# Optimization experiments

Measured on AMD Instinct MI355X. Metric: run time of the kernel, lower is better.

The kernel has to match this reference:

```python
import jax, jax.numpy as jnp
import numpy as np

DIM, M_DIM, FOURIER, KNN = 128, 16, 4, 32
EDGE_IN = 2 * FOURIER + 2 * DIM + 1  # 265


def silu(x):
    return x * jax.nn.sigmoid(x)


def setup_inputs() -> dict:
    key = jax.random.key(0)
    ks = jax.random.split(key, 12)
    b, n = 2, 4096

    def w(k, shape):
        return jax.random.normal(k, shape, dtype=jnp.float32) * 0.02

    return {
        "feats": jax.random.normal(ks[0], (b, n, DIM), dtype=jnp.float32),
        "coors": jax.random.normal(ks[1], (b, n, 3), dtype=jnp.float32) * 3.0,
        # edge_mlp: Linear(265, 530) -> SiLU -> Linear(530, 16) -> SiLU
        "We1": w(ks[2], (EDGE_IN, 2 * EDGE_IN)), "be1": jnp.zeros((2 * EDGE_IN,), jnp.float32),
        "We2": w(ks[3], (2 * EDGE_IN, M_DIM)), "be2": jnp.zeros((M_DIM,), jnp.float32),
        # coors_mlp: Linear(16, 64) -> SiLU -> Linear(64, 1)
        "Wc1": w(ks[4], (M_DIM, 4 * M_DIM)), "bc1": jnp.zeros((4 * M_DIM,), jnp.float32),
        "Wc2": w(ks[5], (4 * M_DIM, 1)), "bc2": jnp.zeros((1,), jnp.float32),
        # node_mlp: Linear(dim+16, 2*dim) -> SiLU -> Linear(2*dim, dim)
        "Wn1": w(ks[6], (DIM + M_DIM, 2 * DIM)), "bn1": jnp.zeros((2 * DIM,), jnp.float32),
        "Wn2": w(ks[7], (2 * DIM, DIM)), "bn2": jnp.zeros((DIM,), jnp.float32),
    }


def reference(feats, coors, We1, be1, We2, be2, Wc1, bc1, Wc2, bc2, Wn1, bn1, Wn2, bn2):
    b, n, d = feats.shape
    # pairwise relative coords and squared distance: (b, n, n, 3), (b, n, n)
    rel_coors = coors[:, :, None, :] - coors[:, None, :, :]
    rel_dist = jnp.sum(rel_coors ** 2, axis=-1)

    # k nearest neighbors (smallest distance)
    _, idx = jax.lax.top_k(-rel_dist, KNN)  # (b, n, K)
    rel_coors = jnp.take_along_axis(rel_coors, idx[..., None], axis=2)  # (b, n, K, 3)
    rel_dist = jnp.take_along_axis(rel_dist, idx, axis=2)[..., None]    # (b, n, K, 1)

    # fourier encode distance -> (b, n, K, 2*F + 1)
    scales = 2.0 ** jnp.arange(FOURIER, dtype=rel_dist.dtype)
    xs = rel_dist[..., None] / scales  # (b, n, K, 1, F)
    fe = jnp.concatenate([jnp.sin(xs), jnp.cos(xs), rel_dist[..., None]], axis=-1)
    rel_dist = fe.reshape(b, n, KNN, 2 * FOURIER + 1)

    bidx = jnp.arange(b)[:, None, None]
    feats_j = feats[bidx, idx]                                   # (b, n, K, d)
    feats_i = jnp.broadcast_to(feats[:, :, None, :], (b, n, KNN, d))

    edge_in = jnp.concatenate([feats_i, feats_j, rel_dist], axis=-1)  # (b, n, K, 265)
    m_ij = silu(silu(edge_in @ We1 + be1) @ We2 + be2)                # (b, n, K, m)

    coor_w = (silu(m_ij @ Wc1 + bc1) @ Wc2 + bc2)[..., 0]             # (b, n, K)
    coors_out = jnp.einsum('bij,bijc->bic', coor_w, rel_coors) + coors

    m_i = m_ij.sum(axis=2)                                            # (b, n, m)
    node_h = silu(jnp.concatenate([feats, m_i], axis=-1) @ Wn1 + bn1)
    node_out = node_h @ Wn2 + bn2 + feats
    return node_out, coors_out
```

## Files before the change

### kernel.cpp

```cpp
#include <hip/hip_runtime.h>
#include <hip/hip_bf16.h>
#include <stdint.h>

typedef __hip_bfloat16 bf16;

using sh8    = __attribute__((ext_vector_type(8)))  short;
using sh4    = __attribute__((ext_vector_type(4)))  short;
using us4    = __attribute__((ext_vector_type(4)))  unsigned short;
using f32x16 = __attribute__((ext_vector_type(16))) float;
using fx4    = __attribute__((ext_vector_type(4)))  float;
using i32x2  = __attribute__((ext_vector_type(2)))  int;

#define NN    4096
#define NODES 8192
#define DIM   128
#define MD    16
#define KNNK  32
#define H1N   530
#define CPAD  544
#define PROW  1088

#define OFF_W1AB 0
#define OFF_WE2A 8704
#define OFF_WC1A 17536
#define OFF_BE2  19584
#define OFF_BC1  19616
#define OFF_WC2  19744
#define OFF_BC2  19872
#define WIMG_SH  19880

__device__ __forceinline__ float b2f(bf16 x){ return __bfloat162float(x); }
__device__ __forceinline__ bf16  f2b(float x){ return __float2bfloat16(x); }
__device__ __forceinline__ float silu_f(float x){
    return x * __builtin_amdgcn_rcpf(1.f + __expf(-x));
}

__device__ __forceinline__ unsigned short f2us(float f){
    unsigned x = __float_as_uint(f);
    unsigned r = x + 0x7FFFu + ((x >> 16) & 1u);
    return (unsigned short)(r >> 16);
}
__device__ __forceinline__ float us2f(unsigned short u){
    return __uint_as_float(((unsigned)u) << 16);
}
__device__ __forceinline__ unsigned pkbf(float a, float b){
    __hip_bfloat162 v = __float22bfloat162_rn(make_float2(a, b));
    return *(unsigned*)&v;
}
__device__ __forceinline__ void plswap(unsigned &a, unsigned &b){
    i32x2 r = __builtin_amdgcn_permlane32_swap((int)a, (int)b, false, false);
    a = (unsigned)r[0]; b = (unsigned)r[1];
}
__device__ __forceinline__ sh8 mk8(unsigned a, unsigned b, unsigned c, unsigned d){
    union { unsigned u[4]; sh8 s; } x;
    x.u[0] = a; x.u[1] = b; x.u[2] = c; x.u[3] = d;
    return x.s;
}
__device__ __forceinline__ float ldconv(const void* p, int fl, size_t i){
    return fl ? ((const float*)p)[i] : b2f(((const bf16*)p)[i]);
}

struct Ptrs { const void* p[14]; int n[14]; };

__global__ __launch_bounds__(256) void detect_kernel(Ptrs ps, int* flags){
    int tn = blockIdx.x;
    const bf16* s = (const bf16*)ps.p[tn];
    int n = ps.n[tn]; if (n > 8192) n = 8192;
    int bad = 0;
    for (int i = threadIdx.x; i < n; i += 256){
        float v = b2f(s[i]);
        if (!(fabsf(v) <= 64.f)) bad = 1;
    }
    __shared__ int sbad;
    if (threadIdx.x == 0) sbad = 0;
    __syncthreads();
    if (bad) atomicOr(&sbad, 1);
    __syncthreads();
    if (threadIdx.x == 0) flags[tn] = sbad;
}

#define PREP_TOTAL 1340352
__global__ __launch_bounds__(256) void prep_all(Ptrs ps, const int* __restrict__ flags,
        unsigned short* __restrict__ gwimg, unsigned short* __restrict__ We1T,
        unsigned short* __restrict__ fBF,   float* __restrict__ coorsF,
        float* __restrict__ be1F,  float* __restrict__ Wn1F,
        float* __restrict__ bn1F,  float* __restrict__ Wn2F,
        float* __restrict__ bn2F,  float* __restrict__ coorsS){
    int gid = blockIdx.x * 256 + threadIdx.x;
    if (gid < 4352){
        int c = gid >> 3, f = gid & 7;
        gwimg[OFF_W1AB + gid] =
            (c < H1N) ? f2us(ldconv(ps.p[2], flags[2], (size_t)(256 + f) * H1N + c)) : 0;
    } else if (gid < 8704){
        int e = gid - 4352; int c = e >> 3, jj = e & 7;
        gwimg[OFF_W1AB + 4352 + e] =
            (jj == 0 && c < H1N) ? f2us(ldconv(ps.p[2], flags[2], (size_t)264 * H1N + c)) : 0;
    } else if (gid < 17536){
        int e = gid - 8704; int o = e / 552, c = e - o * 552;
        gwimg[OFF_WE2A + e] =
            (c < H1N) ? f2us(ldconv(ps.p[4], flags[4], (size_t)c * 16 + o)) : 0;
    } else if (gid < 19584){
        int e = gid - 17536; int u = e >> 5, k = e & 31;
        gwimg[OFF_WC1A + e] =
            (k < 16) ? f2us(ldconv(ps.p[6], flags[6], (size_t)k * 64 + u)) : 0;
    } else if (gid < 19600){
        ((float*)(gwimg + OFF_BE2))[gid - 19584] = ldconv(ps.p[5], flags[5], gid - 19584);
    } else if (gid < 19664){
        ((float*)(gwimg + OFF_BC1))[gid - 19600] = ldconv(ps.p[7], flags[7], gid - 19600);
    } else if (gid < 19728){
        ((float*)(gwimg + OFF_WC2))[gid - 19664] = ldconv(ps.p[8], flags[8], gid - 19664);
    } else if (gid < 19732){
        int z = gid - 19728;
        ((float*)(gwimg + OFF_BC2))[z] = (z == 0) ? ldconv(ps.p[9], flags[9], 0) : 0.f;
    } else if (gid >= 32768 && gid < 172032){
        int e = gid - 32768; int n = e >> 7, k = e & 127;
        float v;
        if (n < CPAD) v = (n < H1N) ? ldconv(ps.p[2], flags[2], (size_t)k * H1N + n) : 0.f;
        else { int n2 = n - CPAD;
               v = (n2 < H1N) ? ldconv(ps.p[2], flags[2], (size_t)(128 + k) * H1N + n2) : 0.f; }
        We1T[e] = f2us(v);
    } else if (gid >= 172032 && gid < 1220608){
        int e = gid - 172032;
        fBF[e] = f2us(ldconv(ps.p[0], flags[0], e));
    } else if (gid >= 1220608 && gid < 1245184){
        int e = gid - 1220608;
        coorsF[e] = ldconv(ps.p[1], flags[1], e);
    } else if (gid >= 1245184 && gid < 1245714){
        int e = gid - 1245184;
        be1F[e] = ldconv(ps.p[3], flags[3], e);
    } else if (gid >= 1245760 && gid < 1282624){
        int e = gid - 1245760;
        Wn1F[e] = ldconv(ps.p[10], flags[10], e);
    } else if (gid >= 1282624 && gid < 1282880){
        int e = gid - 1282624;
        bn1F[e] = ldconv(ps.p[11], flags[11], e);
    } else if (gid >= 1282880 && gid < 1315648){
        int e = gid - 1282880;
        Wn2F[e] = ldconv(ps.p[12], flags[12], e);
    } else if (gid >= 1315648 && gid < 1315776){
        int e = gid - 1315648;
        bn2F[e] = ldconv(ps.p[13], flags[13], e);
    } else if (gid >= 1315776 && gid < 1340352){
        int e = gid - 1315776;
        int n = e / 3, c = e - n * 3;
        coorsS[(size_t)c * NODES + n] = ldconv(ps.p[1], flags[1], e);
    }
}

__global__ __launch_bounds__(512, 6) void knn_kernel(const float* __restrict__ coorsS,
                                                     int* __restrict__ idx_out){
    __shared__ unsigned hist[8][1024];
    __shared__ unsigned long long blist[8][64];
    __shared__ int cntO[8], cntB[8];

    int t = threadIdx.x, lane = t & 63, wid = t >> 6;
    int node = (blockIdx.x << 3) + wid;
    int b = node >> 12, i = node & (NN - 1);
    const float* cx = coorsS + (size_t)b * NN;
    const float* cy = coorsS + NODES + (size_t)b * NN;
    const float* cz = coorsS + 2 * NODES + (size_t)b * NN;

    float qx = cx[i], qy = cy[i], qz = cz[i];

    unsigned* h = &hist[wid][0];
    {
        uint4* hz = (uint4*)h;
        uint4 z = make_uint4(0,0,0,0);
        #pragma unroll
        for (int zl = 0; zl < 4; ++zl) hz[zl * 64 + lane] = z;
    }
    if (lane == 0){ cntO[wid] = 0; cntB[wid] = 0; }
    asm volatile("" ::: "memory");

    for (int s = 0; s < 16; ++s){
        int j0 = (s << 8) + (lane << 2);
        fx4 X = *(const fx4*)(cx + j0);
        fx4 Y = *(const fx4*)(cy + j0);
        fx4 Z = *(const fx4*)(cz + j0);
        #pragma unroll
        for (int k = 0; k < 4; ++k){
            float dx = qx - X[k], dy = qy - Y[k], dz = qz - Z[k];
            float d  = dx*dx + dy*dy + dz*dz;
            float d2 = d * d;
            atomicAdd(&h[__float_as_uint(d2 * d2) >> 22], 1u);
        }
    }
    asm volatile("s_waitcnt lgkmcnt(0)" ::: "memory");

    unsigned S = 0;
    {
        uint4* hz = (uint4*)h;
        #pragma unroll
        for (int g = 0; g < 4; ++g){
            uint4 v = hz[lane * 4 + g];
            S += v.x + v.y + v.z + v.w;
        }
    }
    unsigned scan = S;
    #pragma unroll
    for (int off = 1; off < 64; off <<= 1){
        unsigned nv = __shfl_up(scan, off);
        if (lane >= off) scan += nv;
    }
    unsigned excl = scan - S;
    unsigned long long own = __ballot(excl < KNNK && excl + S >= KNNK);
    int src = __ffsll((unsigned long long)own) - 1;
    unsigned run = excl, Bloc = 0, below_l = 0;
    #pragma unroll
    for (int r = 0; r < 16; ++r){
        unsigned c = h[lane * 16 + r];
        if (run < KNNK && run + c >= KNNK){ Bloc = lane * 16 + r; below_l = run; }
        run += c;
    }
    unsigned B    = __shfl(Bloc, src);
    unsigned below= __shfl(below_l, src);
    unsigned need = KNNK - below;

    int* co = &cntO[wid];
    int* cbn = &cntB[wid];
    unsigned long long* bl = &blist[wid][0];
    for (int s = 0; s < 16; ++s){
        int j0 = (s << 8) + (lane << 2);
        fx4 X = *(const fx4*)(cx + j0);
        fx4 Y = *(const fx4*)(cy + j0);
        fx4 Z = *(const fx4*)(cz + j0);
        #pragma unroll
        for (int k = 0; k < 4; ++k){
            float dx = qx - X[k], dy = qy - Y[k], dz = qz - Z[k];
            float d  = dx*dx + dy*dy + dz*dz;
            float d2 = d * d;
            unsigned bk = __float_as_uint(d2 * d2) >> 22;
            int j = j0 + k;
            if (bk < B){
                int pos = atomicAdd(co, 1);
                idx_out[(size_t)node * KNNK + pos] = j;
            } else if (bk == B){
                unsigned long long mk = ((unsigned long long)__float_as_uint(d) << 32)
                                        | (unsigned)j;
                int p = atomicAdd(cbn, 1);
                if (p < 64) bl[p] = mk;
            }
        }
    }
    asm volatile("s_waitcnt lgkmcnt(0) vmcnt(0)" ::: "memory");
    int nb = *cbn;

    if (nb <= 64){
        unsigned long long e = (lane < nb) ? bl[lane] : ~0ull;
        for (unsigned r = 0; r < need; ++r){
            unsigned long long m = e;
            #pragma unroll
            for (int off = 32; off > 0; off >>= 1){
                unsigned long long o = __shfl_xor(m, off);
                if (o < m) m = o;
            }
            if (lane == 0)
                idx_out[(size_t)node * KNNK + below + r] = (int)(unsigned)(m & 0xffffffffull);
            if (e == m) e = ~0ull;
        }
    } else {
        unsigned long long lastk = 0;
        for (unsigned r = 0; r < need; ++r){
            unsigned long long lmin = ~0ull;
            for (int s = 0; s < 64; ++s){
                int j = (s << 6) + lane;
                float dx = qx - cx[j];
                float dy = qy - cy[j];
                float dz = qz - cz[j];
                float d  = dx*dx + dy*dy + dz*dz;
                float d2 = d * d;
                if ((__float_as_uint(d2 * d2) >> 22) == B){
                    unsigned long long mk = (((unsigned long long)__float_as_uint(d) << 32)
                                             | (unsigned)j) + 1ull;
                    if (mk > lastk && mk < lmin) lmin = mk;
                }
            }
            #pragma unroll
            for (int off = 32; off > 0; off >>= 1){
                unsigned long long o = __shfl_xor(lmin, off);
                if (o < lmin) lmin = o;
            }
            if (lane == 0)
                idx_out[(size_t)node * KNNK + below + r] =
                    (int)(unsigned)((lmin - 1ull) & 0xffffffffull);
            lastk = lmin;
        }
    }
}

__global__ __launch_bounds__(256) void p_gemm(const unsigned short* __restrict__ fBF,
                                              const unsigned short* __restrict__ We1T,
                                              const float* __restrict__ be1,
                                              unsigned short* __restrict__ P){
    int t = threadIdx.x, lane = t & 63, wid = t >> 6;
    int e31 = lane & 31, hi = lane >> 5;
    int mW = (blockIdx.x << 7) + (wid << 5);
    int n0 = blockIdx.y << 5;

    const unsigned short* Arow = fBF  + (size_t)(mW + e31) * DIM + hi * 8;
    const unsigned short* Brow = We1T + (size_t)(n0 + e31) * DIM + hi * 8;

    f32x16 acc = {0.f,0.f,0.f,0.f,0.f,0.f,0.f,0.f,0.f,0.f,0.f,0.f,0.f,0.f,0.f,0.f};
    #pragma unroll
    for (int kc = 0; kc < 8; ++kc){
        sh8 a  = *(const sh8*)(Arow + kc * 16);
        sh8 bv = *(const sh8*)(Brow + kc * 16);
        acc = __builtin_amdgcn_mfma_f32_32x32x16_bf16(a, bv, acc, 0, 0, 0);
    }
    int n = n0 + e31;
    float beadd = 0.f;
    if (n < CPAD) beadd = (n < H1N) ? be1[n] : 0.f;
    #pragma unroll
    for (int g = 0; g < 4; ++g)
        #pragma unroll
        for (int r = 0; r < 4; ++r){
            int m = mW + 8*g + 4*hi + r;
            P[(size_t)m * PROW + n] = f2us(acc[4*g + r] + beadd);
        }
}

__global__ __launch_bounds__(512, 6) void edge_kernel(
        const float* __restrict__ coors, const int* __restrict__ idx,
        const unsigned short* __restrict__ gw,
        const unsigned short* __restrict__ P,
        float* __restrict__ mi_out, void* __restrict__ dout,
        const int* __restrict__ flagp){
    __shared__ __align__(16) unsigned short sWe2[16 * 552];
    __shared__ __align__(16) unsigned short trans[8][1280];

    int t = threadIdx.x, lane = t & 63, wid = t >> 6;
    int gnode = (blockIdx.x << 3) + wid;
    int b = gnode >> 12;

    {
        const float4* s1 = (const float4*)(gw + OFF_WE2A);
        float4* d1 = (float4*)sWe2;
        for (int e = t; e < 1104; e += 512) d1[e] = s1[e];
    }

    const float* cb = coors + (size_t)b * NN * 3;
    int i = gnode & (NN - 1);
    float qx = cb[i*3+0], qy = cb[i*3+1], qz = cb[i*3+2];

    int e31 = lane & 31, hi = lane >> 5;
    int e15 = lane & 15, q  = lane >> 4;

    int jme = idx[(size_t)gnode * KNNK + e31];
    float rx = qx - cb[jme*3+0];
    float ry = qy - cb[jme*3+1];
    float rz = qz - cb[jme*3+2];
    float d = rx*rx + ry*ry + rz*rz;

    float s8v, c8v;
    __sincosf(d * 0.125f, &s8v, &c8v);
    float s4  = 2.f*s8v*c8v, c4  = 1.f - 2.f*s8v*s8v;
    float s2a = 2.f*s4*c4,   c2a = 1.f - 2.f*s4*s4;
    float s1a = 2.f*s2a*c2a, c1a = 1.f - 2.f*s2a*s2a;

    unsigned frb[9];
    frb[0] = f2us(s1a); frb[1] = f2us(s2a); frb[2] = f2us(s4); frb[3] = f2us(s8v);
    frb[4] = f2us(c1a); frb[5] = f2us(c2a); frb[6] = f2us(c4); frb[7] = f2us(c8v);
    frb[8] = f2us(d);

    sh8 bfragC;
    #pragma unroll
    for (int j = 0; j < 8; ++j)
        bfragC[j] = (hi == 0) ? (short)frb[j]
                  : (short)((j == 0) ? frb[8] : (j == 1) ? 0x3F80u : 0u);

    int nbase = gnode & ~(NN - 1);
    int j0 = __shfl(jme, lane >> 2);
    int j1 = __shfl(jme, 16 + (lane >> 2));
    const unsigned short* Pst0 = P + (size_t)(nbase + j0) * PROW + CPAD + (lane & 3) * 8;
    const unsigned short* Pst1 = P + (size_t)(nbase + j1) * PROW + CPAD + (lane & 3) * 8;
    const unsigned short* Pirow = P + (size_t)gnode * PROW;

    unsigned short* stg = &trans[wid][0];
    unsigned short* sw0 = stg + (lane >> 2) * 40 + (lane & 3) * 8;
    unsigned short* sw1 = stg + (16 + (lane >> 2)) * 40 + (lane & 3) * 8;

    const float* g_be2 = (const float*)(gw + OFF_BE2);
    const float* g_bc1 = (const float*)(gw + OFF_BC1);
    const float* g_wc2 = (const float*)(gw + OFF_WC2);
    const float* g_bc2 = (const float*)(gw + OFF_BC2);

    f32x16 accD = {0.f,0.f,0.f,0.f,0.f,0.f,0.f,0.f,
                   0.f,0.f,0.f,0.f,0.f,0.f,0.f,0.f};

    sh8 g0v = *(const sh8*)(Pst0);
    sh8 g1v = *(const sh8*)(Pst1);

    __syncthreads();

    #pragma unroll 1
    for (int ch = 0; ch < 17; ++ch){
        int c0 = ch * 32;
        *(sh8*)sw0 = g0v;
        *(sh8*)sw1 = g1v;
        if (ch < 16){
            g0v = *(const sh8*)(Pst0 + c0 + 32);
            g1v = *(const sh8*)(Pst1 + c0 + 32);
        }

        unsigned short piS = Pirow[c0 + e31];
        sh8 afrag = *(const sh8*)(gw + OFF_W1AB + (size_t)(hi * 544 + c0 + e31) * 8);
        afrag[1] = hi ? (short)piS : afrag[1];

        f32x16 cc;
        #pragma unroll
        for (int g = 0; g < 4; ++g){
            us4 pj = *(const us4*)(stg + e31 * 40 + 8*g + 4*hi);
            cc[4*g+0] = us2f(pj.x);
            cc[4*g+1] = us2f(pj.y);
            cc[4*g+2] = us2f(pj.z);
            cc[4*g+3] = us2f(pj.w);
        }
        f32x16 h = __builtin_amdgcn_mfma_f32_32x32x16_bf16(afrag, bfragC, cc, 0, 0, 0);

        unsigned u0 = pkbf(silu_f(h[0]),  silu_f(h[1]));
        unsigned u1 = pkbf(silu_f(h[2]),  silu_f(h[3]));
        unsigned u2 = pkbf(silu_f(h[4]),  silu_f(h[5]));
        unsigned u3 = pkbf(silu_f(h[6]),  silu_f(h[7]));
        unsigned u4 = pkbf(silu_f(h[8]),  silu_f(h[9]));
        unsigned u5 = pkbf(silu_f(h[10]), silu_f(h[11]));
        unsigned u6 = pkbf(silu_f(h[12]), silu_f(h[13]));
        unsigned u7 = pkbf(silu_f(h[14]), silu_f(h[15]));
        plswap(u0, u2); plswap(u1, u3);
        plswap(u4, u6); plswap(u5, u7);
        sh8 A1 = mk8(u0, u1, u2, u3);
        sh8 A2 = mk8(u4, u5, u6, u7);

        const unsigned short* wrow = &sWe2[(size_t)(e31 & 15) * 552 + c0 + (hi << 3)];
        sh8 B1 = *(const sh8*)(wrow);
        sh8 B2 = *(const sh8*)(wrow + 16);
        accD = __builtin_amdgcn_mfma_f32_32x32x16_bf16(A1, B1, accD, 0, 0, 0);
        accD = __builtin_amdgcn_mfma_f32_32x32x16_bf16(A2, B2, accD, 0, 0, 0);
    }

    float be2v = g_be2[e31 & 15];
    float mval[16];
    float msum = 0.f;
    #pragma unroll
    for (int r = 0; r < 16; ++r){
        mval[r] = silu_f(accD[r] + be2v);
        msum += mval[r];
    }
    msum += __shfl_xor(msum, 32);

    if (e31 < 16){
        #pragma unroll
        for (int r = 0; r < 16; ++r){
            int edge = (r & 3) + 8 * (r >> 2) + 4 * hi;
            stg[edge * 16 + e31] = f2us(mval[r]);
        }
        if (hi == 0)
            mi_out[(size_t)gnode * MD + e31] = msum;
    }

    float tsum0 = 0.f, tsum1 = 0.f;
    #pragma unroll
    for (int ut = 0; ut < 4; ++ut){
        sh8 wa3 = *(const sh8*)(gw + OFF_WC1A + (size_t)(ut * 16 + e15) * 32 + q * 8);
        sh8 b0  = (q < 2) ? *(const sh8*)&stg[e15 * 16 + q * 8]        : (sh8)0;
        sh8 b1  = (q < 2) ? *(const sh8*)&stg[(16 + e15) * 16 + q * 8] : (sh8)0;
        fx4 a0 = {0.f,0.f,0.f,0.f};
        fx4 a1 = {0.f,0.f,0.f,0.f};
        a0 = __builtin_amdgcn_mfma_f32_16x16x32_bf16(wa3, b0, a0, 0, 0, 0);
        a1 = __builtin_amdgcn_mfma_f32_16x16x32_bf16(wa3, b1, a1, 0, 0, 0);
        fx4 bc1q = *(const fx4*)&g_bc1[ut * 16 + q * 4];
        fx4 wcq  = *(const fx4*)&g_wc2[ut * 16 + q * 4];
        #pragma unroll
        for (int r = 0; r < 4; ++r){
            tsum0 += silu_f(a0[r] + bc1q[r]) * wcq[r];
            tsum1 += silu_f(a1[r] + bc1q[r]) * wcq[r];
        }
    }
    tsum0 += __shfl_xor(tsum0, 16); tsum0 += __shfl_xor(tsum0, 32);
    tsum1 += __shfl_xor(tsum1, 16); tsum1 += __shfl_xor(tsum1, 32);
    float cw = ((lane < 16) ? tsum0 : tsum1) + g_bc2[0];

    float en = (lane < 32) ? 1.f : 0.f;
    float cx = en * cw * rx, cy = en * cw * ry, cz = en * cw * rz;
    #pragma unroll
    for (int off = 1; off <= 32; off <<= 1){
        cx += __shfl_xor(cx, off);
        cy += __shfl_xor(cy, off);
        cz += __shfl_xor(cz, off);
    }
    if (lane == 0){
        size_t base = (size_t)NODES * DIM + (size_t)gnode * 3;
        if (*flagp){
            float* o = (float*)dout;
            o[base+0] = cx + qx; o[base+1] = cy + qy; o[base+2] = cz + qz;
        } else {
            bf16* o = (bf16*)dout;
            o[base+0] = f2b(cx + qx); o[base+1] = f2b(cy + qy); o[base+2] = f2b(cz + qz);
        }
    }
}

__global__ __launch_bounds__(256) void node_kernel(
        const void* __restrict__ featsRaw, const float* __restrict__ m_i,
        const float* __restrict__ Wn1,   const float* __restrict__ bn1,
        const float* __restrict__ Wn2,   const float* __restrict__ bn2,
        void* __restrict__ dout,         const int* __restrict__ flagp){
    __shared__ __align__(16) float X[8][144];
    __shared__ __align__(16) float Hs[8][256];
    int t = threadIdx.x;
    int g0 = blockIdx.x << 3;
    int fl = flagp[0];

    for (int e = t; e < 8 * DIM; e += 256){
        int nd = e >> 7, c = e & 127;
        size_t off = (size_t)(g0 + nd) * DIM + c;
        X[nd][c] = fl ? ((const float*)featsRaw)[off]
                      : b2f(((const bf16*)featsRaw)[off]);
    }
    if (t < 128){
        int nd = t >> 4, c = t & 15;
        X[nd][DIM + c] = m_i[(size_t)(g0 + nd) * MD + c];
    }
    __syncthreads();

    float acc[8] = {};
    for (int r4 = 0; r4 < 144; r4 += 4){
        float w0 = Wn1[(size_t)(r4+0) * 256 + t];
        float w1 = Wn1[(size_t)(r4+1) * 256 + t];
        float w2 = Wn1[(size_t)(r4+2) * 256 + t];
        float w3 = Wn1[(size_t)(r4+3) * 256 + t];
        #pragma unroll
        for (int nd = 0; nd < 8; ++nd){
            fx4 x4 = *(const fx4*)&X[nd][r4];
            acc[nd] += x4[0]*w0 + x4[1]*w1 + x4[2]*w2 + x4[3]*w3;
        }
    }
    float bb = bn1[t];
    #pragma unroll
    for (int nd = 0; nd < 8; ++nd) Hs[nd][t] = silu_f(acc[nd] + bb);
    __syncthreads();

    int c = t & 127, g = t >> 7;
    float a2[4] = {};
    for (int r4 = 0; r4 < 256; r4 += 4){
        float w0 = Wn2[(size_t)(r4+0) * DIM + c];
        float w1 = Wn2[(size_t)(r4+1) * DIM + c];
        float w2 = Wn2[(size_t)(r4+2) * DIM + c];
        float w3 = Wn2[(size_t)(r4+3) * DIM + c];
        #pragma unroll
        for (int u = 0; u < 4; ++u){
            fx4 h4 = *(const fx4*)&Hs[g*4 + u][r4];
            a2[u] += h4[0]*w0 + h4[1]*w1 + h4[2]*w2 + h4[3]*w3;
        }
    }
    float b2v = bn2[c];
    #pragma unroll
    for (int u = 0; u < 4; ++u){
        int nd = g*4 + u;
        float v = a2[u] + b2v + X[nd][c];
        size_t off2 = (size_t)(g0 + nd) * DIM + c;
        if (fl) ((float*)dout)[off2] = v;
        else    ((bf16*)dout)[off2]  = f2b(v);
    }
}

extern "C" void kernel_launch(void* const* d_in, const int* in_sizes, int n_in,
                              void* d_out, int out_size, void* d_ws, size_t ws_size,
                              hipStream_t stream){
    char* ws = (char*)d_ws;
    size_t off = 0;
    auto alloc = [&](size_t bytes) -> char* {
        off = (off + 511) & ~(size_t)511;
        char* p = ws + off;
        off += bytes;
        return p;
    };

    int* flags = (int*)alloc(14 * 4);
    unsigned short* gwimg = (unsigned short*)alloc((size_t)WIMG_SH * 2);
    unsigned short* We1T  = (unsigned short*)alloc((size_t)1088 * 128 * 2);
    unsigned short* fBF   = (unsigned short*)alloc((size_t)NODES * DIM * 2);
    float* coorsF = (float*)alloc((size_t)2 * NN * 3 * 4);
    float* be1F   = (float*)alloc((size_t)544 * 4);
    float* Wn1F   = (float*)alloc((size_t)144 * 256 * 4);
    float* bn1F   = (float*)alloc((size_t)256 * 4);
    float* Wn2F   = (float*)alloc((size_t)256 * 128 * 4);
    float* bn2F   = (float*)alloc((size_t)128 * 4);
    float* coorsS = (float*)alloc((size_t)3 * NODES * 4);
    int*   idx    = (int*)  alloc((size_t)NODES * KNNK * 4);
    unsigned short* P = (unsigned short*) alloc((size_t)NODES * PROW * 2);
    float* mi     = (float*)alloc((size_t)NODES * MD * 4);

    Ptrs ps;
    for (int i = 0; i < 14; ++i){ ps.p[i] = d_in[i]; ps.n[i] = in_sizes[i]; }

    detect_kernel<<<14, 256, 0, stream>>>(ps, flags);
    prep_all<<<(PREP_TOTAL + 255) / 256, 256, 0, stream>>>(
        ps, flags, gwimg, We1T, fBF, coorsF, be1F, Wn1F, bn1F, Wn2F, bn2F, coorsS);
    knn_kernel<<<NODES/8, 512, 0, stream>>>(coorsS, idx);
    p_gemm<<<dim3(64, 34), 256, 0, stream>>>(fBF, We1T, be1F, P);
    edge_kernel<<<NODES/8, 512, 0, stream>>>(coorsF, idx, gwimg, P, mi,
                                             d_out, flags + 0);
    node_kernel<<<1024, 256, 0, stream>>>(d_in[0], mi, Wn1F, bn1F, Wn2F, bn2F,
                                          d_out, flags + 0);
}
```

Measured before the change: 252.0 us.

## Merge knn with P-gemm and fuse node MLP into edge kernel

Folds the independent P-projection GEMM into the knn launch as extra blocks, so both run concurrently in one grid. It also fuses the node MLP into the edge kernel epilogue, keeping per-node message sums in shared memory instead of a global m_i buffer. Together these remove two launches and a global round trip. The cost is more shared memory and extra work per edge block, which may lower occupancy. The GEMM blocks also inherit the knn kernel's 512-thread launch bounds and shared-memory allocation.

```diff
diff --git a/kernel.cpp b/kernel.cpp
--- a/kernel.cpp
+++ b/kernel.cpp
@@ -147,14 +147,49 @@
     }
 }
 
-__global__ __launch_bounds__(512, 6) void knn_kernel(const float* __restrict__ coorsS,
-                                                     int* __restrict__ idx_out){
+__global__ __launch_bounds__(512, 6) void knn_pgemm(
+        const float* __restrict__ coorsS, int* __restrict__ idx_out,
+        const unsigned short* __restrict__ fBF,
+        const unsigned short* __restrict__ We1T,
+        const float* __restrict__ be1, unsigned short* __restrict__ P){
     __shared__ unsigned hist[8][1024];
     __shared__ unsigned long long blist[8][64];
     __shared__ int cntO[8], cntB[8];
 
+    int bid = blockIdx.x;
     int t = threadIdx.x, lane = t & 63, wid = t >> 6;
-    int node = (blockIdx.x << 3) + wid;
+    int e31 = lane & 31, hi = lane >> 5;
+
+    if (bid >= 1024){
+        int sub = bid - 1024;
+        int bx = sub & 63, by = sub >> 6;
+        int mW = (bx << 7) + ((wid & 3) << 5);
+        int n0 = (by << 6) + ((wid >> 2) << 5);
+
+        const unsigned short* Arow = fBF  + (size_t)(mW + e31) * DIM + hi * 8;
+        const unsigned short* Brow = We1T + (size_t)(n0 + e31) * DIM + hi * 8;
+
+        f32x16 acc = {0.f,0.f,0.f,0.f,0.f,0.f,0.f,0.f,0.f,0.f,0.f,0.f,0.f,0.f,0.f,0.f};
+        #pragma unroll
+        for (int kc = 0; kc < 8; ++kc){
+            sh8 a  = *(const sh8*)(Arow + kc * 16);
+            sh8 bv = *(const sh8*)(Brow + kc * 16);
+            acc = __builtin_amdgcn_mfma_f32_32x32x16_bf16(a, bv, acc, 0, 0, 0);
+        }
+        int n = n0 + e31;
+        float beadd = 0.f;
+        if (n < CPAD) beadd = (n < H1N) ? be1[n] : 0.f;
+        #pragma unroll
+        for (int g = 0; g < 4; ++g)
+            #pragma unroll
+            for (int r = 0; r < 4; ++r){
+                int m = mW + 8*g + 4*hi + r;
+                P[(size_t)m * PROW + n] = f2us(acc[4*g + r] + beadd);
+            }
+        return;
+    }
+
+    int node = (bid << 3) + wid;
     int b = node >> 12, i = node & (NN - 1);
     const float* cx = coorsS + (size_t)b * NN;
     const float* cy = coorsS + NODES + (size_t)b * NN;
@@ -288,54 +323,37 @@
     }
 }
 
-__global__ __launch_bounds__(256) void p_gemm(const unsigned short* __restrict__ fBF,
-                                              const unsigned short* __restrict__ We1T,
-                                              const float* __restrict__ be1,
-                                              unsigned short* __restrict__ P){
-    int t = threadIdx.x, lane = t & 63, wid = t >> 6;
-    int e31 = lane & 31, hi = lane >> 5;
-    int mW = (blockIdx.x << 7) + (wid << 5);
-    int n0 = blockIdx.y << 5;
-
-    const unsigned short* Arow = fBF  + (size_t)(mW + e31) * DIM + hi * 8;
-    const unsigned short* Brow = We1T + (size_t)(n0 + e31) * DIM + hi * 8;
-
-    f32x16 acc = {0.f,0.f,0.f,0.f,0.f,0.f,0.f,0.f,0.f,0.f,0.f,0.f,0.f,0.f,0.f,0.f};
-    #pragma unroll
-    for (int kc = 0; kc < 8; ++kc){
-        sh8 a  = *(const sh8*)(Arow + kc * 16);
-        sh8 bv = *(const sh8*)(Brow + kc * 16);
-        acc = __builtin_amdgcn_mfma_f32_32x32x16_bf16(a, bv, acc, 0, 0, 0);
-    }
-    int n = n0 + e31;
-    float beadd = 0.f;
-    if (n < CPAD) beadd = (n < H1N) ? be1[n] : 0.f;
-    #pragma unroll
-    for (int g = 0; g < 4; ++g)
-        #pragma unroll
-        for (int r = 0; r < 4; ++r){
-            int m = mW + 8*g + 4*hi + r;
-            P[(size_t)m * PROW + n] = f2us(acc[4*g + r] + beadd);
-        }
-}
-
-__global__ __launch_bounds__(512, 6) void edge_kernel(
+__global__ __launch_bounds__(512, 6) void edge_node(
         const float* __restrict__ coors, const int* __restrict__ idx,
         const unsigned short* __restrict__ gw,
         const unsigned short* __restrict__ P,
-        float* __restrict__ mi_out, void* __restrict__ dout,
-        const int* __restrict__ flagp){
+        const void* __restrict__ featsRaw,
+        const float* __restrict__ Wn1,  const float* __restrict__ bn1,
+        const float* __restrict__ Wn2,  const float* __restrict__ bn2,
+        void* __restrict__ dout,        const int* __restrict__ flagp){
     __shared__ __align__(16) unsigned short sWe2[16 * 552];
     __shared__ __align__(16) unsigned short trans[8][1280];
+    __shared__ __align__(16) float Xn[8][144];
+    __shared__ __align__(16) float Hsn[8][256];
 
     int t = threadIdx.x, lane = t & 63, wid = t >> 6;
     int gnode = (blockIdx.x << 3) + wid;
+    int gblk  = blockIdx.x << 3;
     int b = gnode >> 12;
+    int fl = flagp[0];
 
     {
         const float4* s1 = (const float4*)(gw + OFF_WE2A);
         float4* d1 = (float4*)sWe2;
         for (int e = t; e < 1104; e += 512) d1[e] = s1[e];
+    }
+    {
+        for (int e = t; e < 8 * DIM; e += 512){
+            int nd = e >> 7, c = e & 127;
+            size_t off = (size_t)(gblk + nd) * DIM + c;
+            Xn[nd][c] = fl ? ((const float*)featsRaw)[off]
+                           : b2f(((const bf16*)featsRaw)[off]);
+        }
     }
 
     const float* cb = coors + (size_t)b * NN * 3;
@@ -454,7 +472,7 @@
             stg[edge * 16 + e31] = f2us(mval[r]);
         }
         if (hi == 0)
-            mi_out[(size_t)gnode * MD + e31] = msum;
+            Xn[wid][DIM + e31] = msum;
     }
 
     float tsum0 = 0.f, tsum1 = 0.f;
@@ -480,86 +498,68 @@
     float cw = ((lane < 16) ? tsum0 : tsum1) + g_bc2[0];
 
     float en = (lane < 32) ? 1.f : 0.f;
-    float cx = en * cw * rx, cy = en * cw * ry, cz = en * cw * rz;
+    float cxo = en * cw * rx, cyo = en * cw * ry, czo = en * cw * rz;
     #pragma unroll
     for (int off = 1; off <= 32; off <<= 1){
-        cx += __shfl_xor(cx, off);
-        cy += __shfl_xor(cy, off);
-        cz += __shfl_xor(cz, off);
+        cxo += __shfl_xor(cxo, off);
+        cyo += __shfl_xor(cyo, off);
+        czo += __shfl_xor(czo, off);
     }
     if (lane == 0){
         size_t base = (size_t)NODES * DIM + (size_t)gnode * 3;
-        if (*flagp){
+        if (fl){
             float* o = (float*)dout;
-            o[base+0] = cx + qx; o[base+1] = cy + qy; o[base+2] = cz + qz;
+            o[base+0] = cxo + qx; o[base+1] = cyo + qy; o[base+2] = czo + qz;
         } else {
             bf16* o = (bf16*)dout;
-            o[base+0] = f2b(cx + qx); o[base+1] = f2b(cy + qy); o[base+2] = f2b(cz + qz);
-        }
-    }
-}
-
-__global__ __launch_bounds__(256) void node_kernel(
-        const void* __restrict__ featsRaw, const float* __restrict__ m_i,
-        const float* __restrict__ Wn1,   const float* __restrict__ bn1,
-        const float* __restrict__ Wn2,   const float* __restrict__ bn2,
-        void* __restrict__ dout,         const int* __restrict__ flagp){
-    __shared__ __align__(16) float X[8][144];
-    __shared__ __align__(16) float Hs[8][256];
-    int t = threadIdx.x;
-    int g0 = blockIdx.x << 3;
-    int fl = flagp[0];
-
-    for (int e = t; e < 8 * DIM; e += 256){
-        int nd = e >> 7, c = e & 127;
-        size_t off = (size_t)(g0 + nd) * DIM + c;
-        X[nd][c] = fl ? ((const float*)featsRaw)[off]
-                      : b2f(((const bf16*)featsRaw)[off]);
-    }
-    if (t < 128){
-        int nd = t >> 4, c = t & 15;
-        X[nd][DIM + c] = m_i[(size_t)(g0 + nd) * MD + c];
-    }
+            o[base+0] = f2b(cxo + qx); o[base+1] = f2b(cyo + qy); o[base+2] = f2b(czo + qz);
+        }
+    }
+
     __syncthreads();
 
-    float acc[8] = {};
-    for (int r4 = 0; r4 < 144; r4 += 4){
-        float w0 = Wn1[(size_t)(r4+0) * 256 + t];
-        float w1 = Wn1[(size_t)(r4+1) * 256 + t];
-        float w2 = Wn1[(size_t)(r4+2) * 256 + t];
-        float w3 = Wn1[(size_t)(r4+3) * 256 + t];
-        #pragma unroll
-        for (int nd = 0; nd < 8; ++nd){
-            fx4 x4 = *(const fx4*)&X[nd][r4];
-            acc[nd] += x4[0]*w0 + x4[1]*w1 + x4[2]*w2 + x4[3]*w3;
-        }
-    }
-    float bb = bn1[t];
-    #pragma unroll
-    for (int nd = 0; nd < 8; ++nd) Hs[nd][t] = silu_f(acc[nd] + bb);
+    {
+        int c8 = t & 255, g2 = t >> 8;
+        float accN[4] = {};
+        for (int r4 = 0; r4 < 144; r4 += 4){
+            float w0 = Wn1[(size_t)(r4+0) * 256 + c8];
+            float w1 = Wn1[(size_t)(r4+1) * 256 + c8];
+            float w2 = Wn1[(size_t)(r4+2) * 256 + c8];
+            float w3 = Wn1[(size_t)(r4+3) * 256 + c8];
+            #pragma unroll
+            for (int u = 0; u < 4; ++u){
+                fx4 x4 = *(const fx4*)&Xn[g2*4 + u][r4];
+                accN[u] += x4[0]*w0 + x4[1]*w1 + x4[2]*w2 + x4[3]*w3;
+            }
+        }
+        float bb = bn1[c8];
+        #pragma unroll
+        for (int u = 0; u < 4; ++u) Hsn[g2*4 + u][c8] = silu_f(accN[u] + bb);
+    }
     __syncthreads();
-
-    int c = t & 127, g = t >> 7;
-    float a2[4] = {};
-    for (int r4 = 0; r4 < 256; r4 += 4){
-        float w0 = Wn2[(size_t)(r4+0) * DIM + c];
-        float w1 = Wn2[(size_t)(r4+1) * DIM + c];
-        float w2 = Wn2[(size_t)(r4+2) * DIM + c];
-        float w3 = Wn2[(size_t)(r4+3) * DIM + c];
-        #pragma unroll
-        for (int u = 0; u < 4; ++u){
-            fx4 h4 = *(const fx4*)&Hs[g*4 + u][r4];
-            a2[u] += h4[0]*w0 + h4[1]*w1 + h4[2]*w2 + h4[3]*w3;
-        }
-    }
-    float b2v = bn2[c];
-    #pragma unroll
-    for (int u = 0; u < 4; ++u){
-        int nd = g*4 + u;
-        float v = a2[u] + b2v + X[nd][c];
-        size_t off2 = (size_t)(g0 + nd) * DIM + c;
-        if (fl) ((float*)dout)[off2] = v;
-        else    ((bf16*)dout)[off2]  = f2b(v);
+    {
+        int c7 = t & 127, g3 = t >> 7;
+        float a2[2] = {};
+        for (int r4 = 0; r4 < 256; r4 += 4){
+            float w0 = Wn2[(size_t)(r4+0) * DIM + c7];
+            float w1 = Wn2[(size_t)(r4+1) * DIM + c7];
+            float w2 = Wn2[(size_t)(r4+2) * DIM + c7];
+            float w3 = Wn2[(size_t)(r4+3) * DIM + c7];
+            #pragma unroll
+            for (int u = 0; u < 2; ++u){
+                fx4 h4 = *(const fx4*)&Hsn[g3*2 + u][r4];
+                a2[u] += h4[0]*w0 + h4[1]*w1 + h4[2]*w2 + h4[3]*w3;
+            }
+        }
+        float b2v = bn2[c7];
+        #pragma unroll
+        for (int u = 0; u < 2; ++u){
+            int nd = g3*2 + u;
+            float v = a2[u] + b2v + Xn[nd][c7];
+            size_t off2 = (size_t)(gblk + nd) * DIM + c7;
+            if (fl) ((float*)dout)[off2] = v;
+            else    ((bf16*)dout)[off2]  = f2b(v);
+        }
     }
 }
 
@@ -588,7 +588,6 @@
     float* coorsS = (float*)alloc((size_t)3 * NODES * 4);
     int*   idx    = (int*)  alloc((size_t)NODES * KNNK * 4);
     unsigned short* P = (unsigned short*) alloc((size_t)NODES * PROW * 2);
-    float* mi     = (float*)alloc((size_t)NODES * MD * 4);
 
     Ptrs ps;
     for (int i = 0; i < 14; ++i){ ps.p[i] = d_in[i]; ps.n[i] = in_sizes[i]; }
@@ -596,10 +595,8 @@
     detect_kernel<<<14, 256, 0, stream>>>(ps, flags);
     prep_all<<<(PREP_TOTAL + 255) / 256, 256, 0, stream>>>(
         ps, flags, gwimg, We1T, fBF, coorsF, be1F, Wn1F, bn1F, Wn2F, bn2F, coorsS);
-    knn_kernel<<<NODES/8, 512, 0, stream>>>(coorsS, idx);
-    p_gemm<<<dim3(64, 34), 256, 0, stream>>>(fBF, We1T, be1F, P);
-    edge_kernel<<<NODES/8, 512, 0, stream>>>(coorsF, idx, gwimg, P, mi,
-                                             d_out, flags + 0);
-    node_kernel<<<1024, 256, 0, stream>>>(d_in[0], mi, Wn1F, bn1F, Wn2F, bn2F,
-                                          d_out, flags + 0);
-}
+    knn_pgemm<<<2112, 512, 0, stream>>>(coorsS, idx, fBF, We1T, be1F, P);
+    edge_node<<<NODES/8, 512, 0, stream>>>(coorsF, idx, gwimg, P, d_in[0],
+                                           Wn1F, bn1F, Wn2F, bn2F,
+                                           d_out, flags + 0);
+}
```

Result: no change. 256.8 us (+1.9%).

## Fuse KNN selection into edge kernel and swizzle staging LDS layout

Applied to the files above, without the earlier changes.

Merges the KNN selection into the edge kernel so each wave computes its 32 neighbour indices into shared memory and uses them directly, removing the idx global buffer and one launch. The histogram and edge staging buffers share LDS through a union to keep occupancy. It also XOR-swizzles the transpose staging buffer addresses to reduce LDS bank conflicts. The cost is a longer fused kernel with higher register pressure, and the KNN phase can no longer overlap with p_gemm.

```diff
diff --git a/kernel.cpp b/kernel.cpp
--- a/kernel.cpp
+++ b/kernel.cpp
@@ -147,147 +147,6 @@
     }
 }
 
-__global__ __launch_bounds__(512, 6) void knn_kernel(const float* __restrict__ coorsS,
-                                                     int* __restrict__ idx_out){
-    __shared__ unsigned hist[8][1024];
-    __shared__ unsigned long long blist[8][64];
-    __shared__ int cntO[8], cntB[8];
-
-    int t = threadIdx.x, lane = t & 63, wid = t >> 6;
-    int node = (blockIdx.x << 3) + wid;
-    int b = node >> 12, i = node & (NN - 1);
-    const float* cx = coorsS + (size_t)b * NN;
-    const float* cy = coorsS + NODES + (size_t)b * NN;
-    const float* cz = coorsS + 2 * NODES + (size_t)b * NN;
-
-    float qx = cx[i], qy = cy[i], qz = cz[i];
-
-    unsigned* h = &hist[wid][0];
-    {
-        uint4* hz = (uint4*)h;
-        uint4 z = make_uint4(0,0,0,0);
-        #pragma unroll
-        for (int zl = 0; zl < 4; ++zl) hz[zl * 64 + lane] = z;
-    }
-    if (lane == 0){ cntO[wid] = 0; cntB[wid] = 0; }
-    asm volatile("" ::: "memory");
-
-    for (int s = 0; s < 16; ++s){
-        int j0 = (s << 8) + (lane << 2);
-        fx4 X = *(const fx4*)(cx + j0);
-        fx4 Y = *(const fx4*)(cy + j0);
-        fx4 Z = *(const fx4*)(cz + j0);
-        #pragma unroll
-        for (int k = 0; k < 4; ++k){
-            float dx = qx - X[k], dy = qy - Y[k], dz = qz - Z[k];
-            float d  = dx*dx + dy*dy + dz*dz;
-            float d2 = d * d;
-            atomicAdd(&h[__float_as_uint(d2 * d2) >> 22], 1u);
-        }
-    }
-    asm volatile("s_waitcnt lgkmcnt(0)" ::: "memory");
-
-    unsigned S = 0;
-    {
-        uint4* hz = (uint4*)h;
-        #pragma unroll
-        for (int g = 0; g < 4; ++g){
-            uint4 v = hz[lane * 4 + g];
-            S += v.x + v.y + v.z + v.w;
-        }
-    }
-    unsigned scan = S;
-    #pragma unroll
-    for (int off = 1; off < 64; off <<= 1){
-        unsigned nv = __shfl_up(scan, off);
-        if (lane >= off) scan += nv;
-    }
-    unsigned excl = scan - S;
-    unsigned long long own = __ballot(excl < KNNK && excl + S >= KNNK);
-    int src = __ffsll((unsigned long long)own) - 1;
-    unsigned run = excl, Bloc = 0, below_l = 0;
-    #pragma unroll
-    for (int r = 0; r < 16; ++r){
-        unsigned c = h[lane * 16 + r];
-        if (run < KNNK && run + c >= KNNK){ Bloc = lane * 16 + r; below_l = run; }
-        run += c;
-    }
-    unsigned B    = __shfl(Bloc, src);
-    unsigned below= __shfl(below_l, src);
-    unsigned need = KNNK - below;
-
-    int* co = &cntO[wid];
-    int* cbn = &cntB[wid];
-    unsigned long long* bl = &blist[wid][0];
-    for (int s = 0; s < 16; ++s){
-        int j0 = (s << 8) + (lane << 2);
-        fx4 X = *(const fx4*)(cx + j0);
-        fx4 Y = *(const fx4*)(cy + j0);
-        fx4 Z = *(const fx4*)(cz + j0);
-        #pragma unroll
-        for (int k = 0; k < 4; ++k){
-            float dx = qx - X[k], dy = qy - Y[k], dz = qz - Z[k];
-            float d  = dx*dx + dy*dy + dz*dz;
-            float d2 = d * d;
-            unsigned bk = __float_as_uint(d2 * d2) >> 22;
-            int j = j0 + k;
-            if (bk < B){
-                int pos = atomicAdd(co, 1);
-                idx_out[(size_t)node * KNNK + pos] = j;
-            } else if (bk == B){
-                unsigned long long mk = ((unsigned long long)__float_as_uint(d) << 32)
-                                        | (unsigned)j;
-                int p = atomicAdd(cbn, 1);
-                if (p < 64) bl[p] = mk;
-            }
-        }
-    }
-    asm volatile("s_waitcnt lgkmcnt(0) vmcnt(0)" ::: "memory");
-    int nb = *cbn;
-
-    if (nb <= 64){
-        unsigned long long e = (lane < nb) ? bl[lane] : ~0ull;
-        for (unsigned r = 0; r < need; ++r){
-            unsigned long long m = e;
-            #pragma unroll
-            for (int off = 32; off > 0; off >>= 1){
-                unsigned long long o = __shfl_xor(m, off);
-                if (o < m) m = o;
-            }
-            if (lane == 0)
-                idx_out[(size_t)node * KNNK + below + r] = (int)(unsigned)(m & 0xffffffffull);
-            if (e == m) e = ~0ull;
-        }
-    } else {
-        unsigned long long lastk = 0;
-        for (unsigned r = 0; r < need; ++r){
-            unsigned long long lmin = ~0ull;
-            for (int s = 0; s < 64; ++s){
-                int j = (s << 6) + lane;
-                float dx = qx - cx[j];
-                float dy = qy - cy[j];
-                float dz = qz - cz[j];
-                float d  = dx*dx + dy*dy + dz*dz;
-                float d2 = d * d;
-                if ((__float_as_uint(d2 * d2) >> 22) == B){
-                    unsigned long long mk = (((unsigned long long)__float_as_uint(d) << 32)
-                                             | (unsigned)j) + 1ull;
-                    if (mk > lastk && mk < lmin) lmin = mk;
-                }
-            }
-            #pragma unroll
-            for (int off = 32; off > 0; off >>= 1){
-                unsigned long long o = __shfl_xor(lmin, off);
-                if (o < lmin) lmin = o;
-            }
-            if (lane == 0)
-                idx_out[(size_t)node * KNNK + below + r] =
-                    (int)(unsigned)((lmin - 1ull) & 0xffffffffull);
-            lastk = lmin;
-        }
-    }
-}
-
 __global__ __launch_bounds__(256) void p_gemm(const unsigned short* __restrict__ fBF,
                                               const unsigned short* __restrict__ We1T,
                                               const float* __restrict__ be1,
@@ -319,33 +178,172 @@
         }
 }
 
-__global__ __launch_bounds__(512, 6) void edge_kernel(
-        const float* __restrict__ coors, const int* __restrict__ idx,
+__global__ __launch_bounds__(512, 6) void edge_knn(
+        const float* __restrict__ coorsF, const float* __restrict__ coorsS,
         const unsigned short* __restrict__ gw,
         const unsigned short* __restrict__ P,
         float* __restrict__ mi_out, void* __restrict__ dout,
         const int* __restrict__ flagp){
-    __shared__ __align__(16) unsigned short sWe2[16 * 552];
-    __shared__ __align__(16) unsigned short trans[8][1280];
+    __shared__ __align__(16) union ShU {
+        struct { unsigned hist[8][1024]; unsigned long long blist[8][64]; } k;
+        struct { unsigned short sWe2[16*552]; unsigned short trans[8][1280]; } e;
+    } sh;
+    __shared__ int idxw[8][32];
+    __shared__ int cntO[8], cntB[8];
 
     int t = threadIdx.x, lane = t & 63, wid = t >> 6;
     int gnode = (blockIdx.x << 3) + wid;
     int b = gnode >> 12;
+    int e31 = lane & 31, hi = lane >> 5;
+    int e15 = lane & 15, q  = lane >> 4;
+
+    {
+        int i = gnode & (NN - 1);
+        const float* cx = coorsS + (size_t)b * NN;
+        const float* cy = coorsS + NODES + (size_t)b * NN;
+        const float* cz = coorsS + 2 * NODES + (size_t)b * NN;
+
+        float qx = cx[i], qy = cy[i], qz = cz[i];
+
+        unsigned* h = &sh.k.hist[wid][0];
+        {
+            uint4* hz = (uint4*)h;
+            uint4 z = make_uint4(0,0,0,0);
+            #pragma unroll
+            for (int zl = 0; zl < 4; ++zl) hz[zl * 64 + lane] = z;
+        }
+        if (lane == 0){ cntO[wid] = 0; cntB[wid] = 0; }
+        asm volatile("" ::: "memory");
+
+        for (int s = 0; s < 16; ++s){
+            int j0 = (s << 8) + (lane << 2);
+            fx4 X = *(const fx4*)(cx + j0);
+            fx4 Y = *(const fx4*)(cy + j0);
+            fx4 Z = *(const fx4*)(cz + j0);
+            #pragma unroll
+            for (int k = 0; k < 4; ++k){
+                float dx = qx - X[k], dy = qy - Y[k], dz = qz - Z[k];
+                float d  = dx*dx + dy*dy + dz*dz;
+                float d2 = d * d;
+                atomicAdd(&h[__float_as_uint(d2 * d2) >> 22], 1u);
+            }
+        }
+        asm volatile("s_waitcnt lgkmcnt(0)" ::: "memory");
+
+        unsigned S = 0;
+        {
+            uint4* hz = (uint4*)h;
+            #pragma unroll
+            for (int g = 0; g < 4; ++g){
+                uint4 v = hz[lane * 4 + g];
+                S += v.x + v.y + v.z + v.w;
+            }
+        }
+        unsigned scan = S;
+        #pragma unroll
+        for (int off = 1; off < 64; off <<= 1){
+            unsigned nv = __shfl_up(scan, off);
+            if (lane >= off) scan += nv;
+        }
+        unsigned excl = scan - S;
+        unsigned long long own = __ballot(excl < KNNK && excl + S >= KNNK);
+        int src = __ffsll((unsigned long long)own) - 1;
+        unsigned run = excl, Bloc = 0, below_l = 0;
+        #pragma unroll
+        for (int r = 0; r < 16; ++r){
+            unsigned c = h[lane * 16 + r];
+            if (run < KNNK && run + c >= KNNK){ Bloc = lane * 16 + r; below_l = run; }
+            run += c;
+        }
+        unsigned B    = __shfl(Bloc, src);
+        unsigned below= __shfl(below_l, src);
+        unsigned need = KNNK - below;
+
+        int* co = &cntO[wid];
+        int* cbn = &cntB[wid];
+        unsigned long long* bl = &sh.k.blist[wid][0];
+        int* iw = &idxw[wid][0];
+        for (int s = 0; s < 16; ++s){
+            int j0 = (s << 8) + (lane << 2);
+            fx4 X = *(const fx4*)(cx + j0);
+            fx4 Y = *(const fx4*)(cy + j0);
+            fx4 Z = *(const fx4*)(cz + j0);
+            #pragma unroll
+            for (int k = 0; k < 4; ++k){
+                float dx = qx - X[k], dy = qy - Y[k], dz = qz - Z[k];
+                float d  = dx*dx + dy*dy + dz*dz;
+                float d2 = d * d;
+                unsigned bk = __float_as_uint(d2 * d2) >> 22;
+                int j = j0 + k;
+                if (bk < B){
+                    int pos = atomicAdd(co, 1);
+                    iw[pos] = j;
+                } else if (bk == B){
+                    unsigned long long mk = ((unsigned long long)__float_as_uint(d) << 32)
+                                            | (unsigned)j;
+                    int p = atomicAdd(cbn, 1);
+                    if (p < 64) bl[p] = mk;
+                }
+            }
+        }
+        asm volatile("s_waitcnt lgkmcnt(0) vmcnt(0)" ::: "memory");
+        int nb = *cbn;
+
+        if (nb <= 64){
+            unsigned long long e = (lane < nb) ? bl[lane] : ~0ull;
+            for (unsigned r = 0; r < need; ++r){
+                unsigned long long m = e;
+                #pragma unroll
+                for (int off = 32; off > 0; off >>= 1){
+                    unsigned long long o = __shfl_xor(m, off);
+                    if (o < m) m = o;
+                }
+                if (lane == 0)
+                    iw[below + r] = (int)(unsigned)(m & 0xffffffffull);
+                if (e == m) e = ~0ull;
+            }
+        } else {
+            unsigned long long lastk = 0;
+            for (unsigned r = 0; r < need; ++r){
+                unsigned long long lmin = ~0ull;
+                for (int s = 0; s < 64; ++s){
+                    int j = (s << 6) + lane;
+                    float dx = qx - cx[j];
+                    float dy = qy - cy[j];
+                    float dz = qz - cz[j];
+                    float d  = dx*dx + dy*dy + dz*dz;
+                    float d2 = d * d;
+                    if ((__float_as_uint(d2 * d2) >> 22) == B){
+                        unsigned long long mk = (((unsigned long long)__float_as_uint(d) << 32)
+                                                 | (unsigned)j) + 1ull;
+                        if (mk > lastk && mk < lmin) lmin = mk;
+                    }
+                }
+                #pragma unroll
+                for (int off = 32; off > 0; off >>= 1){
+                    unsigned long long o = __shfl_xor(lmin, off);
+                    if (o < lmin) lmin = o;
+                }
+                if (lane == 0)
+                    iw[below + r] = (int)(unsigned)((lmin - 1ull) & 0xffffffffull);
+                lastk = lmin;
+            }
+        }
+    }
+
+    __syncthreads();
 
     {
         const float4* s1 = (const float4*)(gw + OFF_WE2A);
-        float4* d1 = (float4*)sWe2;
+        float4* d1 = (float4*)sh.e.sWe2;
         for (int e = t; e < 1104; e += 512) d1[e] = s1[e];
     }
 
-    const float* cb = coors + (size_t)b * NN * 3;
+    const float* cb = coorsF + (size_t)b * NN * 3;
     int i = gnode & (NN - 1);
     float qx = cb[i*3+0], qy = cb[i*3+1], qz = cb[i*3+2];
 
-    int e31 = lane & 31, hi = lane >> 5;
-    int e15 = lane & 15, q  = lane >> 4;
-
-    int jme = idx[(size_t)gnode * KNNK + e31];
+    int jme = idxw[wid][e31];
     float rx = qx - cb[jme*3+0];
     float ry = qy - cb[jme*3+1];
     float rz = qz - cb[jme*3+2];
@@ -375,9 +373,11 @@
     const unsigned short* Pst1 = P + (size_t)(nbase + j1) * PROW + CPAD + (lane & 3) * 8;
     const unsigned short* Pirow = P + (size_t)gnode * PROW;
 
-    unsigned short* stg = &trans[wid][0];
-    unsigned short* sw0 = stg + (lane >> 2) * 40 + (lane & 3) * 8;
-    unsigned short* sw1 = stg + (16 + (lane >> 2)) * 40 + (lane & 3) * 8;
+    unsigned short* stg = &sh.e.trans[wid][0];
+    {   }
+    int r0 = lane >> 2, r1 = 16 + (lane >> 2), qq = lane & 3;
+    unsigned short* sw0 = stg + r0 * 40 + ((qq ^ (r0 >> 3)) << 3);
+    unsigned short* sw1 = stg + r1 * 40 + ((qq ^ (r1 >> 3)) << 3);
 
     const float* g_be2 = (const float*)(gw + OFF_BE2);
     const float* g_bc1 = (const float*)(gw + OFF_BC1);
@@ -389,6 +389,9 @@
 
     sh8 g0v = *(const sh8*)(Pst0);
     sh8 g1v = *(const sh8*)(Pst1);
+
+    int sx = e31 >> 3;
+    const unsigned short* ccb = stg + e31 * 40 + 4 * hi;
 
     __syncthreads();
 
@@ -409,7 +412,7 @@
         f32x16 cc;
         #pragma unroll
         for (int g = 0; g < 4; ++g){
-            us4 pj = *(const us4*)(stg + e31 * 40 + 8*g + 4*hi);
+            us4 pj = *(const us4*)(ccb + ((g ^ sx) << 3));
             cc[4*g+0] = us2f(pj.x);
             cc[4*g+1] = us2f(pj.y);
             cc[4*g+2] = us2f(pj.z);
@@ -430,7 +433,7 @@
         sh8 A1 = mk8(u0, u1, u2, u3);
         sh8 A2 = mk8(u4, u5, u6, u7);
 
-        const unsigned short* wrow = &sWe2[(size_t)(e31 & 15) * 552 + c0 + (hi << 3)];
+        const unsigned short* wrow = &sh.e.sWe2[(size_t)(e31 & 15) * 552 + c0 + (hi << 3)];
         sh8 B1 = *(const sh8*)(wrow);
         sh8 B2 = *(const sh8*)(wrow + 16);
         accD = __builtin_amdgcn_mfma_f32_32x32x16_bf16(A1, B1, accD, 0, 0, 0);
@@ -480,21 +483,21 @@
     float cw = ((lane < 16) ? tsum0 : tsum1) + g_bc2[0];
 
     float en = (lane < 32) ? 1.f : 0.f;
-    float cx = en * cw * rx, cy = en * cw * ry, cz = en * cw * rz;
+    float cx2 = en * cw * rx, cy2 = en * cw * ry, cz2 = en * cw * rz;
     #pragma unroll
     for (int off = 1; off <= 32; off <<= 1){
-        cx += __shfl_xor(cx, off);
-        cy += __shfl_xor(cy, off);
-        cz += __shfl_xor(cz, off);
+        cx2 += __shfl_xor(cx2, off);
+        cy2 += __shfl_xor(cy2, off);
+        cz2 += __shfl_xor(cz2, off);
     }
     if (lane == 0){
         size_t base = (size_t)NODES * DIM + (size_t)gnode * 3;
         if (*flagp){
             float* o = (float*)dout;
-            o[base+0] = cx + qx; o[base+1] = cy + qy; o[base+2] = cz + qz;
+            o[base+0] = cx2 + qx; o[base+1] = cy2 + qy; o[base+2] = cz2 + qz;
         } else {
             bf16* o = (bf16*)dout;
-            o[base+0] = f2b(cx + qx); o[base+1] = f2b(cy + qy); o[base+2] = f2b(cz + qz);
+            o[base+0] = f2b(cx2 + qx); o[base+1] = f2b(cy2 + qy); o[base+2] = f2b(cz2 + qz);
         }
     }
 }
@@ -586,7 +589,6 @@
     float* Wn2F   = (float*)alloc((size_t)256 * 128 * 4);
     float* bn2F   = (float*)alloc((size_t)128 * 4);
     float* coorsS = (float*)alloc((size_t)3 * NODES * 4);
-    int*   idx    = (int*)  alloc((size_t)NODES * KNNK * 4);
     unsigned short* P = (unsigned short*) alloc((size_t)NODES * PROW * 2);
     float* mi     = (float*)alloc((size_t)NODES * MD * 4);
 
@@ -596,10 +598,9 @@
     detect_kernel<<<14, 256, 0, stream>>>(ps, flags);
     prep_all<<<(PREP_TOTAL + 255) / 256, 256, 0, stream>>>(
         ps, flags, gwimg, We1T, fBF, coorsF, be1F, Wn1F, bn1F, Wn2F, bn2F, coorsS);
-    knn_kernel<<<NODES/8, 512, 0, stream>>>(coorsS, idx);
     p_gemm<<<dim3(64, 34), 256, 0, stream>>>(fBF, We1T, be1F, P);
-    edge_kernel<<<NODES/8, 512, 0, stream>>>(coorsF, idx, gwimg, P, mi,
-                                             d_out, flags + 0);
+    edge_knn<<<NODES/8, 512, 0, stream>>>(coorsF, coorsS, gwimg, P, mi,
+                                          d_out, flags + 0);
     node_kernel<<<1024, 256, 0, stream>>>(d_in[0], mi, Wn1F, bn1F, Wn2F, bn2F,
                                           d_out, flags + 0);
 }
```

Measured after the change: 251.0 us. Within noise of the previous version (-0.4%).
